# Optimization experiments

Hardware: AMD Instinct MI355X
Metric: run time of the kernel (lower is better)

The kernel has to match this reference:

```python
import jax, jax.numpy as jnp
import numpy as np

EMBED = 1024
HEADS = 16
HEAD_DIM = EMBED // HEADS
N, L = 8, 1024


def setup_inputs() -> dict:
    key = jax.random.key(0)
    ks = jax.random.split(key, 12)
    s = 1.0 / np.sqrt(EMBED)
    return {
        "values": jax.random.normal(ks[0], (N, L, EMBED), jnp.float32),
        "keys": jax.random.normal(ks[1], (N, L, EMBED), jnp.float32),
        "queries": jax.random.normal(ks[2], (N, L, EMBED), jnp.float32),
        "mask": jax.random.randint(ks[3], (N, 1, L, L), 0, 2, jnp.int32),
        "Wv": jax.random.normal(ks[4], (EMBED, EMBED), jnp.float32) * s,
        "bv": jnp.zeros((EMBED,), jnp.float32),
        "Wk": jax.random.normal(ks[5], (EMBED, EMBED), jnp.float32) * s,
        "bk": jnp.zeros((EMBED,), jnp.float32),
        "Wq": jax.random.normal(ks[6], (EMBED, EMBED), jnp.float32) * s,
        "bq": jnp.zeros((EMBED,), jnp.float32),
        "Wo": jax.random.normal(ks[7], (EMBED, EMBED), jnp.float32) * s,
        "bo": jnp.zeros((EMBED,), jnp.float32),
    }


def reference(values, keys, queries, mask, Wv, bv, Wk, bk, Wq, bq, Wo, bo):
    n, q_len = queries.shape[0], queries.shape[1]
    # Linear projections (torch Linear: x @ W.T + b)
    v = values @ Wv.T + bv
    k = keys @ Wk.T + bk
    q = queries @ Wq.T + bq
    # split heads: [N, L, H, D]
    v = v.reshape(n, -1, HEADS, HEAD_DIM)
    k = k.reshape(n, -1, HEADS, HEAD_DIM)
    q = q.reshape(n, q_len, HEADS, HEAD_DIM)
    # energy: [N, H, Q, K]
    energy = jnp.einsum("nqhd,nkhd->nhqk", q, k)
    energy = jnp.where(mask == 0, jnp.float32(-1e20), energy)
    attention = jax.nn.softmax(energy / jnp.sqrt(jnp.float32(EMBED)), axis=3)
    out = jnp.einsum("nhqk,nkhd->nqhd", attention, v).reshape(n, q_len, EMBED)
    return out @ Wo.T + bo
```

## Files before the change

### kernel.cpp

```cpp
#include <hip/hip_runtime.h>
#include <hip/hip_bf16.h>


typedef __attribute__((ext_vector_type(8))) short short8;
typedef __attribute__((ext_vector_type(8))) __bf16 bf16x8;
typedef __attribute__((ext_vector_type(4))) float f32x4;
typedef __attribute__((ext_vector_type(16))) float f32x16;
typedef __attribute__((ext_vector_type(4))) unsigned short ushort4v;

static __device__ __forceinline__ unsigned short f2bf(float x) {
  union { float f; unsigned u; } v; v.f = x;
  unsigned r = v.u + 0x7FFFu + ((v.u >> 16) & 1u);
  return (unsigned short)(r >> 16);
}

static __device__ __forceinline__ f32x4 mfma16(short8 a, short8 b, f32x4 c) {
  return __builtin_amdgcn_mfma_f32_16x16x32_bf16(
      __builtin_bit_cast(bf16x8, a), __builtin_bit_cast(bf16x8, b), c, 0, 0, 0);
}
static __device__ __forceinline__ f32x16 mfma32(short8 a, short8 b, f32x16 c) {
  return __builtin_amdgcn_mfma_f32_32x32x16_bf16(
      __builtin_bit_cast(bf16x8, a), __builtin_bit_cast(bf16x8, b), c, 0, 0, 0);
}

static __device__ __forceinline__ void gll16(const unsigned short* g, unsigned short* l) {
  __builtin_amdgcn_global_load_lds(
      (const __attribute__((address_space(1))) unsigned int*)(const void*)g,
      (__attribute__((address_space(3))) unsigned int*)(void*)l, 16, 0, 0);
}

static __device__ __forceinline__ unsigned cvtpk(float lo, float hi) {
  unsigned r;
  asm("v_cvt_pk_bf16_f32 %0, %1, %2" : "=v"(r) : "v"(lo), "v"(hi));
  return r;
}

static __device__ __forceinline__ void cvt8(const float* __restrict__ in,
                                            unsigned short* __restrict__ out, int i) {
  float4 a = ((const float4*)in)[i * 2];
  float4 b = ((const float4*)in)[i * 2 + 1];
  union { short8 v; unsigned short u[8]; } pk;
  pk.u[0] = f2bf(a.x); pk.u[1] = f2bf(a.y); pk.u[2] = f2bf(a.z); pk.u[3] = f2bf(a.w);
  pk.u[4] = f2bf(b.x); pk.u[5] = f2bf(b.y); pk.u[6] = f2bf(b.z); pk.u[7] = f2bf(b.w);
  ((short8*)out)[i] = pk.v;
}

__global__ __launch_bounds__(256)
void fused_pre(const float* __restrict__ queries, const float* __restrict__ keys,
               const float* __restrict__ Wq, const float* __restrict__ Wk,
               const float* __restrict__ Wv, const float* __restrict__ Wo,
               const int* __restrict__ mask,
               unsigned short* __restrict__ Xq, unsigned short* __restrict__ Xk,
               unsigned short* __restrict__ W4, unsigned long long* __restrict__ M64)
{
  const int bid = blockIdx.x, tid = threadIdx.x;
  if (bid < 4096) {
    cvt8(queries, Xq, bid * 256 + tid);
  } else if (bid < 8192) {
    cvt8(keys, Xk, (bid - 4096) * 256 + tid);
  } else if (bid < 10240) {
    const int wsel = (bid - 8192) >> 9;
    const float* src = wsel == 0 ? Wq : wsel == 1 ? Wk : wsel == 2 ? Wv : Wo;
    cvt8(src, W4 + wsel * 1048576, ((bid - 8192) & 511) * 256 + tid);
  } else {
    const int lane = tid & 63, wid = tid >> 6;
    const int gw = (bid - 10240) * 4 + wid;
#pragma unroll 4
    for (int j = 0; j < 32; ++j) {
      const int w = gw * 32 + j;
      unsigned long long b = __ballot(mask[(size_t)w * 64 + lane] != 0);
      if (lane == 0) M64[w] = b;
    }
  }
}

__global__ __launch_bounds__(256)
void cvt_kernel(const float* __restrict__ in, unsigned short* __restrict__ out, int n8)
{
  int i = blockIdx.x * 256 + threadIdx.x;
  if (i >= n8) return;
  cvt8(in, out, i);
}

template<int MODE>
__global__ __launch_bounds__(256)
void gemm_kernel(const unsigned short* __restrict__ A, const unsigned short* __restrict__ B,
                 const float* __restrict__ bias, void* __restrict__ outp)
{
  __shared__ alignas(16) unsigned short As[128][32];
  __shared__ alignas(16) unsigned short Bs[128][32];
  const int tid = threadIdx.x, lane = tid & 63, wid = tid >> 6;
  const int l15 = lane & 15, lg = lane >> 4;
  const int bm = blockIdx.x >> 3, bn = blockIdx.x & 7;
  const int wr = (wid >> 1) * 64, wc = (wid & 1) * 64;

  f32x4 acc[4][4] = {};
  const int o = wid * 1024 + lane * 16;
  const unsigned short* gA0 = A + (size_t)(bm * 128 + (o >> 6)) * 1024 + ((o & 63) >> 1);
  const unsigned short* gA1 = gA0 + 64 * 1024;
  const unsigned short* gB0 = B + (size_t)(bn * 128 + (o >> 6)) * 1024 + ((o & 63) >> 1);
  const unsigned short* gB1 = gB0 + 64 * 1024;
  unsigned short* lA0 = &As[0][0] + wid * 512;
  unsigned short* lA1 = lA0 + 2048;
  unsigned short* lB0 = &Bs[0][0] + wid * 512;
  unsigned short* lB1 = lB0 + 2048;

  for (int k0 = 0; k0 < 1024; k0 += 32) {
    __syncthreads();
    gll16(gA0 + k0, lA0); gll16(gA1 + k0, lA1);
    gll16(gB0 + k0, lB0); gll16(gB1 + k0, lB1);
    __syncthreads();
    short8 af[4], bf[4];
#pragma unroll
    for (int f = 0; f < 4; ++f) {
      af[f] = *(const short8*)&As[wr + f * 16 + l15][lg * 8];
      bf[f] = *(const short8*)&Bs[wc + f * 16 + l15][lg * 8];
    }
#pragma unroll
    for (int r = 0; r < 4; ++r)
#pragma unroll
      for (int c = 0; c < 4; ++c)
        acc[r][c] = mfma16(af[r], bf[c], acc[r][c]);
  }

#pragma unroll
  for (int r = 0; r < 4; ++r) {
    const int mb = bm * 128 + wr + r * 16 + lg * 4;
#pragma unroll
    for (int c = 0; c < 4; ++c) {
      const int col = bn * 128 + wc + c * 16 + l15;
      const float bv = bias[col];
      if (MODE == 0) {
        unsigned short* O = (unsigned short*)outp;
#pragma unroll
        for (int i = 0; i < 4; ++i)
          O[(size_t)(mb + i) * 1024 + col] = f2bf(acc[r][c][i] + bv);
      } else if (MODE == 1) {
        unsigned short* O = (unsigned short*)outp;
        const int n = mb >> 10, l = mb & 1023, hh = col >> 6, d = col & 63;
        union { ushort4v v; unsigned short u[4]; } pk;
#pragma unroll
        for (int i = 0; i < 4; ++i) pk.u[i] = f2bf(acc[r][c][i] + bv);
        *(ushort4v*)&O[(size_t)((n * 16 + hh) * 64 + d) * 1024 + l] = pk.v;
      } else {
        float* O = (float*)outp;
#pragma unroll
        for (int i = 0; i < 4; ++i)
          O[(size_t)(mb + i) * 1024 + col] = acc[r][c][i] + bv;
      }
    }
  }
}

__global__ __launch_bounds__(256)
void attn_kernel(const unsigned short* __restrict__ Q,
                 const unsigned short* __restrict__ K,
                 const unsigned short* __restrict__ VT,
                 const unsigned long long* __restrict__ M64,
                 unsigned short* __restrict__ AO)
{
  __shared__ alignas(16) unsigned short KV[2][8192];
  const int tid = threadIdx.x, lane = tid & 63, wid = tid >> 6;
  const int l31 = lane & 31, hi = lane >> 5, hi4 = hi * 4;
  const int w = (blockIdx.x & 7) * 128 + (blockIdx.x >> 3);
  const int qt = w & 7, nh = w >> 3, h = nh & 15, n = nh >> 4;
  const int qbase = qt * 128 + wid * 32;

  const unsigned short* src[4];
  unsigned short* dst0[4];
  int tstride;
  if (wid < 2) {
#pragma unroll
    for (int i = 0; i < 4; ++i) {
      const int g = wid * 4 + i, c = g >> 1, kh = g & 1;
      src[i] = K + ((size_t)(n * 1024 + kh * 32 + l31) << 10) + h * 64 + c * 16 + hi * 8;
      dst0[i] = &KV[0][g * 512];
    }
    tstride = 64 * 1024;
  } else {
#pragma unroll
    for (int i = 0; i < 4; ++i) {
      const int g = (wid - 2) * 4 + i, kt = g >> 1, dh = g & 1;
      src[i] = VT + ((size_t)((n * 16 + h) * 64 + dh * 32 + l31) << 10) + kt * 16 + hi * 8;
      dst0[i] = &KV[0][4096 + g * 512];
    }
    tstride = 64;
  }

  short8 qf[4];
#pragma unroll
  for (int c = 0; c < 4; ++c)
    qf[c] = *(const short8*)&Q[(size_t)(n * 1024 + qbase + l31) * 1024 + h * 64 + c * 16 + hi * 8];

  const unsigned long long* Mq = M64 + (size_t)(n * 1024 + qbase + l31) * 16;
  unsigned long long mw = Mq[0], mwn = 0;

  f32x16 oacc0 = {}, oacc1 = {}, lacc = {};
  const float SC = 0.03125f * 1.44269504089f;
  short8 ones;
#pragma unroll
  for (int j = 0; j < 8; ++j) ones[j] = (short)0x3F80;

#pragma unroll
  for (int i = 0; i < 4; ++i) gll16(src[i], dst0[i]);

  int cur = 0;
#pragma unroll 2
  for (int t = 0; t < 16; ++t) {
    __syncthreads();
    if (t < 15) {
      const size_t off = (size_t)(t + 1) * tstride;
#pragma unroll
      for (int i = 0; i < 4; ++i) gll16(src[i] + off, dst0[i] + (cur ^ 1) * 8192);
      mwn = Mq[t + 1];
    }
    const unsigned short* Kb = &KV[cur][0];

    f32x16 s0 = {}, s1 = {};
#pragma unroll
    for (int c = 0; c < 4; ++c) {
      short8 kf0 = *(const short8*)&Kb[(c * 2 + 0) * 512 + lane * 8];
      short8 kf1 = *(const short8*)&Kb[(c * 2 + 1) * 512 + lane * 8];
      s0 = mfma32(kf0, qf[c], s0);
      s1 = mfma32(kf1, qf[c], s1);
    }

    const unsigned wlo = (unsigned)mw >> hi4;
    const unsigned whi = (unsigned)(mw >> 32) >> hi4;
    short8 pa[4];
#pragma unroll
    for (int kt = 0; kt < 2; ++kt) {
      const unsigned wsh = kt ? whi : wlo;
      float p[16];
#pragma unroll
      for (int r = 0; r < 16; ++r) {
        const float pe = exp2f((kt ? s1[r] : s0[r]) * SC);
        const int pos = 8 * (r >> 2) + (r & 3);
        const int msk = ((int)(wsh << (31 - pos))) >> 31;
        p[r] = __builtin_bit_cast(float, __builtin_bit_cast(int, pe) & msk);
      }
      unsigned u[4][2];
#pragma unroll
      for (int g = 0; g < 4; ++g) {
        u[g][0] = cvtpk(p[4 * g], p[4 * g + 1]);
        u[g][1] = cvtpk(p[4 * g + 2], p[4 * g + 3]);
      }
#pragma unroll
      for (int m = 0; m < 2; ++m) {
        unsigned a0 = u[2 * m][0], b0 = u[2 * m + 1][0];
        unsigned a1 = u[2 * m][1], b1 = u[2 * m + 1][1];
        asm("v_permlane32_swap_b32 %0, %1" : "+v"(a0), "+v"(b0));
        asm("v_permlane32_swap_b32 %0, %1" : "+v"(a1), "+v"(b1));
        union { unsigned uu[4]; short8 v; } pk;
        pk.uu[0] = a0; pk.uu[1] = a1; pk.uu[2] = b0; pk.uu[3] = b1;
        pa[kt * 2 + m] = pk.v;
      }
    }

#pragma unroll
    for (int kt = 0; kt < 4; ++kt) {
      short8 vf0 = *(const short8*)&Kb[4096 + (kt * 2 + 0) * 512 + lane * 8];
      short8 vf1 = *(const short8*)&Kb[4096 + (kt * 2 + 1) * 512 + lane * 8];
      oacc0 = mfma32(pa[kt], vf0, oacc0);
      oacc1 = mfma32(pa[kt], vf1, oacc1);
      lacc  = mfma32(pa[kt], ones, lacc);
    }

    mw = mwn;
    cur ^= 1;
  }

#pragma unroll
  for (int r = 0; r < 16; ++r) {
    const int qrow = 8 * (r >> 2) + (r & 3) + hi4;
    const float rl = 1.0f / lacc[r];
    const size_t row = (size_t)(n * 1024 + qbase + qrow) * 1024 + h * 64;
    AO[row + l31]      = f2bf(oacc0[r] * rl);
    AO[row + 32 + l31] = f2bf(oacc1[r] * rl);
  }
}

extern "C" void kernel_launch(void* const* d_in, const int* in_sizes, int n_in,
                              void* d_out, int out_size, void* d_ws, size_t ws_size,
                              hipStream_t stream) {
  (void)in_sizes; (void)n_in; (void)out_size; (void)ws_size;
  const float* values  = (const float*)d_in[0];
  const float* keys    = (const float*)d_in[1];
  const float* queries = (const float*)d_in[2];
  const int*   mask    = (const int*)d_in[3];
  const float* Wv = (const float*)d_in[4];
  const float* bv = (const float*)d_in[5];
  const float* Wk = (const float*)d_in[6];
  const float* bk = (const float*)d_in[7];
  const float* Wq = (const float*)d_in[8];
  const float* bq = (const float*)d_in[9];
  const float* Wo = (const float*)d_in[10];
  const float* bo = (const float*)d_in[11];

  const size_t MB = 1u << 20;
  char* ws = (char*)d_ws;
  unsigned short* R0  = (unsigned short*)(ws);
  unsigned short* R16 = (unsigned short*)(ws + 16 * MB);
  unsigned short* Qb  = (unsigned short*)(ws + 32 * MB);
  unsigned short* Kb  = (unsigned short*)(ws + 48 * MB);
  unsigned short* W4  = (unsigned short*)(ws + 64 * MB);
  unsigned long long* M64 = (unsigned long long*)(ws + 72 * MB);

  const dim3 b256(256);
  const int NX8 = 8 * 1024 * 1024 / 8;

  fused_pre<<<dim3(11264), b256, 0, stream>>>(queries, keys, Wq, Wk, Wv, Wo, mask,
                                              R0, R16, W4, M64);
  gemm_kernel<0><<<dim3(512), b256, 0, stream>>>(R0,  W4,               bq, (void*)Qb);
  gemm_kernel<0><<<dim3(512), b256, 0, stream>>>(R16, W4 + 1048576,     bk, (void*)Kb);
  cvt_kernel<<<dim3(4096), b256, 0, stream>>>(values, R0, NX8);
  gemm_kernel<1><<<dim3(512), b256, 0, stream>>>(R0,  W4 + 2 * 1048576, bv, (void*)R16);
  attn_kernel<<<dim3(1024), b256, 0, stream>>>(Qb, Kb, R16, M64, R0 );
  gemm_kernel<2><<<dim3(512), b256, 0, stream>>>(R0,  W4 + 3 * 1048576, bo, d_out);
}
```

Before: 231.3 us.

## Pipeline attention PV with next QK, fold scale into Q, fuse values cvt

The attention loop is software-pipelined. The PV MFMAs for the previous tile run after the QK MFMAs of the current tile, with a triple-buffered V LDS ring and s_setprio hints. The row-sum MFMA against a ones vector is replaced by scalar per-lane sums combined with a shuffle and a bpermute. The softmax scale is folded into the Q projection epilogue, the values conversion moves into the fused preprocessing kernel when the workspace is large enough, and the GEMM block order is swizzled for L2 reuse. These changes add register pressure from the double-buffered probability fragments, and rounding differs slightly because the scale is applied before bf16 conversion.

After: 325.9 us. 40.9% more time.

```diff
diff --git a/kernel.cpp b/kernel.cpp
--- a/kernel.cpp
+++ b/kernel.cpp
@@ -47,10 +47,12 @@
 
 __global__ __launch_bounds__(256)
 void fused_pre(const float* __restrict__ queries, const float* __restrict__ keys,
+               const float* __restrict__ values,
                const float* __restrict__ Wq, const float* __restrict__ Wk,
                const float* __restrict__ Wv, const float* __restrict__ Wo,
                const int* __restrict__ mask,
                unsigned short* __restrict__ Xq, unsigned short* __restrict__ Xk,
+               unsigned short* __restrict__ Xv,
                unsigned short* __restrict__ W4, unsigned long long* __restrict__ M64)
 {
   const int bid = blockIdx.x, tid = threadIdx.x;
@@ -62,7 +64,7 @@
     const int wsel = (bid - 8192) >> 9;
     const float* src = wsel == 0 ? Wq : wsel == 1 ? Wk : wsel == 2 ? Wv : Wo;
     cvt8(src, W4 + wsel * 1048576, ((bid - 8192) & 511) * 256 + tid);
-  } else {
+  } else if (bid < 11264) {
     const int lane = tid & 63, wid = tid >> 6;
     const int gw = (bid - 10240) * 4 + wid;
 #pragma unroll 4
@@ -71,6 +73,8 @@
       unsigned long long b = __ballot(mask[(size_t)w * 64 + lane] != 0);
       if (lane == 0) M64[w] = b;
     }
+  } else {
+    cvt8(values, Xv, (bid - 11264) * 256 + tid);
   }
 }
 
@@ -85,13 +89,14 @@
 template<int MODE>
 __global__ __launch_bounds__(256)
 void gemm_kernel(const unsigned short* __restrict__ A, const unsigned short* __restrict__ B,
-                 const float* __restrict__ bias, void* __restrict__ outp)
+                 const float* __restrict__ bias, void* __restrict__ outp, float oscale)
 {
   __shared__ alignas(16) unsigned short As[128][32];
   __shared__ alignas(16) unsigned short Bs[128][32];
   const int tid = threadIdx.x, lane = tid & 63, wid = tid >> 6;
   const int l15 = lane & 15, lg = lane >> 4;
-  const int bm = blockIdx.x >> 3, bn = blockIdx.x & 7;
+  const int j = blockIdx.x >> 3;
+  const int bm = (blockIdx.x & 7) * 8 + (j & 7), bn = j >> 3;
   const int wr = (wid >> 1) * 64, wc = (wid & 1) * 64;
 
   f32x4 acc[4][4] = {};
@@ -134,7 +139,7 @@
         unsigned short* O = (unsigned short*)outp;
 #pragma unroll
         for (int i = 0; i < 4; ++i)
-          O[(size_t)(mb + i) * 1024 + col] = f2bf(acc[r][c][i] + bv);
+          O[(size_t)(mb + i) * 1024 + col] = f2bf((acc[r][c][i] + bv) * oscale);
       } else if (MODE == 1) {
         unsigned short* O = (unsigned short*)outp;
         const int n = mb >> 10, l = mb & 1023, hh = col >> 6, d = col & 63;
@@ -159,7 +164,8 @@
                  const unsigned long long* __restrict__ M64,
                  unsigned short* __restrict__ AO)
 {
-  __shared__ alignas(16) unsigned short KV[2][8192];
+  __shared__ alignas(16) unsigned short Kb[2][4096];
+  __shared__ alignas(16) unsigned short Vb[3][4096];
   const int tid = threadIdx.x, lane = tid & 63, wid = tid >> 6;
   const int l31 = lane & 31, hi = lane >> 5, hi4 = hi * 4;
   const int w = (blockIdx.x & 7) * 128 + (blockIdx.x >> 3);
@@ -167,24 +173,25 @@
   const int qbase = qt * 128 + wid * 32;
 
   const unsigned short* src[4];
-  unsigned short* dst0[4];
-  int tstride;
-  if (wid < 2) {
+  int ldsoff[4];
+  size_t tstep;
+  const bool isK = wid < 2;
+  if (isK) {
 #pragma unroll
     for (int i = 0; i < 4; ++i) {
       const int g = wid * 4 + i, c = g >> 1, kh = g & 1;
       src[i] = K + ((size_t)(n * 1024 + kh * 32 + l31) << 10) + h * 64 + c * 16 + hi * 8;
-      dst0[i] = &KV[0][g * 512];
-    }
-    tstride = 64 * 1024;
+      ldsoff[i] = g * 512;
+    }
+    tstep = 64 * 1024;
   } else {
 #pragma unroll
     for (int i = 0; i < 4; ++i) {
       const int g = (wid - 2) * 4 + i, kt = g >> 1, dh = g & 1;
-      src[i] = VT + ((size_t)((n * 16 + h) * 64 + dh * 32 + l31) << 10) + kt * 16 + hi * 8;
-      dst0[i] = &KV[0][4096 + g * 512];
-    }
-    tstride = 64;
+      src[i] = VT + ((size_t)(nh * 64 + dh * 32 + l31) << 10) + kt * 16 + hi * 8;
+      ldsoff[i] = g * 512;
+    }
+    tstep = 64;
   }
 
   short8 qf[4];
@@ -195,50 +202,63 @@
   const unsigned long long* Mq = M64 + (size_t)(n * 1024 + qbase + l31) * 16;
   unsigned long long mw = Mq[0], mwn = 0;
 
-  f32x16 oacc0 = {}, oacc1 = {}, lacc = {};
-  const float SC = 0.03125f * 1.44269504089f;
-  short8 ones;
-#pragma unroll
-  for (int j = 0; j < 8; ++j) ones[j] = (short)0x3F80;
-
-#pragma unroll
-  for (int i = 0; i < 4; ++i) gll16(src[i], dst0[i]);
-
-  int cur = 0;
-#pragma unroll 2
+  f32x16 oacc0 = {}, oacc1 = {};
+  float l_r = 0.f;
+  short8 pa[2][4];
+
+  {
+    unsigned short* base = isK ? &Kb[0][0] : &Vb[0][0];
+#pragma unroll
+    for (int i = 0; i < 4; ++i) gll16(src[i], base + ldsoff[i]);
+  }
+
+#pragma unroll
   for (int t = 0; t < 16; ++t) {
     __syncthreads();
     if (t < 15) {
-      const size_t off = (size_t)(t + 1) * tstride;
-#pragma unroll
-      for (int i = 0; i < 4; ++i) gll16(src[i] + off, dst0[i] + (cur ^ 1) * 8192);
+      unsigned short* base = isK ? &Kb[(t + 1) & 1][0] : &Vb[(t + 1) % 3][0];
+      const size_t off = (size_t)(t + 1) * tstep;
+#pragma unroll
+      for (int i = 0; i < 4; ++i) gll16(src[i] + off, base + ldsoff[i]);
       mwn = Mq[t + 1];
     }
-    const unsigned short* Kb = &KV[cur][0];
 
     f32x16 s0 = {}, s1 = {};
+    __builtin_amdgcn_s_setprio(1);
 #pragma unroll
     for (int c = 0; c < 4; ++c) {
-      short8 kf0 = *(const short8*)&Kb[(c * 2 + 0) * 512 + lane * 8];
-      short8 kf1 = *(const short8*)&Kb[(c * 2 + 1) * 512 + lane * 8];
+      short8 kf0 = *(const short8*)&Kb[t & 1][(c * 2 + 0) * 512 + lane * 8];
+      short8 kf1 = *(const short8*)&Kb[t & 1][(c * 2 + 1) * 512 + lane * 8];
       s0 = mfma32(kf0, qf[c], s0);
       s1 = mfma32(kf1, qf[c], s1);
     }
+    if (t > 0) {
+#pragma unroll
+      for (int kt = 0; kt < 4; ++kt) {
+        short8 vf0 = *(const short8*)&Vb[(t - 1) % 3][(kt * 2 + 0) * 512 + lane * 8];
+        short8 vf1 = *(const short8*)&Vb[(t - 1) % 3][(kt * 2 + 1) * 512 + lane * 8];
+        oacc0 = mfma32(pa[(t - 1) & 1][kt], vf0, oacc0);
+        oacc1 = mfma32(pa[(t - 1) & 1][kt], vf1, oacc1);
+      }
+    }
+    __builtin_amdgcn_s_setprio(0);
 
     const unsigned wlo = (unsigned)mw >> hi4;
     const unsigned whi = (unsigned)(mw >> 32) >> hi4;
-    short8 pa[4];
 #pragma unroll
     for (int kt = 0; kt < 2; ++kt) {
       const unsigned wsh = kt ? whi : wlo;
       float p[16];
+      float lsum = 0.f;
 #pragma unroll
       for (int r = 0; r < 16; ++r) {
-        const float pe = exp2f((kt ? s1[r] : s0[r]) * SC);
+        const float pe = exp2f(kt ? s1[r] : s0[r]);
         const int pos = 8 * (r >> 2) + (r & 3);
         const int msk = ((int)(wsh << (31 - pos))) >> 31;
         p[r] = __builtin_bit_cast(float, __builtin_bit_cast(int, pe) & msk);
-      }
+        lsum += p[r];
+      }
+      l_r += lsum;
       unsigned u[4][2];
 #pragma unroll
       for (int g = 0; g < 4; ++g) {
@@ -253,27 +273,29 @@
         asm("v_permlane32_swap_b32 %0, %1" : "+v"(a1), "+v"(b1));
         union { unsigned uu[4]; short8 v; } pk;
         pk.uu[0] = a0; pk.uu[1] = a1; pk.uu[2] = b0; pk.uu[3] = b1;
-        pa[kt * 2 + m] = pk.v;
-      }
-    }
-
-#pragma unroll
-    for (int kt = 0; kt < 4; ++kt) {
-      short8 vf0 = *(const short8*)&Kb[4096 + (kt * 2 + 0) * 512 + lane * 8];
-      short8 vf1 = *(const short8*)&Kb[4096 + (kt * 2 + 1) * 512 + lane * 8];
-      oacc0 = mfma32(pa[kt], vf0, oacc0);
-      oacc1 = mfma32(pa[kt], vf1, oacc1);
-      lacc  = mfma32(pa[kt], ones, lacc);
-    }
-
+        pa[t & 1][kt * 2 + m] = pk.v;
+      }
+    }
     mw = mwn;
-    cur ^= 1;
-  }
-
+  }
+
+  __builtin_amdgcn_s_setprio(1);
+#pragma unroll
+  for (int kt = 0; kt < 4; ++kt) {
+    short8 vf0 = *(const short8*)&Vb[0][(kt * 2 + 0) * 512 + lane * 8];
+    short8 vf1 = *(const short8*)&Vb[0][(kt * 2 + 1) * 512 + lane * 8];
+    oacc0 = mfma32(pa[1][kt], vf0, oacc0);
+    oacc1 = mfma32(pa[1][kt], vf1, oacc1);
+  }
+  __builtin_amdgcn_s_setprio(0);
+
+  const float l_tot = l_r + __shfl_xor(l_r, 32);
+  const float inv_l = 1.0f / l_tot;
+  const int invi = __builtin_bit_cast(int, inv_l);
 #pragma unroll
   for (int r = 0; r < 16; ++r) {
     const int qrow = 8 * (r >> 2) + (r & 3) + hi4;
-    const float rl = 1.0f / lacc[r];
+    const float rl = __builtin_bit_cast(float, __builtin_amdgcn_ds_bpermute(qrow * 4, invi));
     const size_t row = (size_t)(n * 1024 + qbase + qrow) * 1024 + h * 64;
     AO[row + l31]      = f2bf(oacc0[r] * rl);
     AO[row + 32 + l31] = f2bf(oacc1[r] * rl);
@@ -283,7 +305,7 @@
 extern "C" void kernel_launch(void* const* d_in, const int* in_sizes, int n_in,
                               void* d_out, int out_size, void* d_ws, size_t ws_size,
                               hipStream_t stream) {
-  (void)in_sizes; (void)n_in; (void)out_size; (void)ws_size;
+  (void)in_sizes; (void)n_in; (void)out_size;
   const float* values  = (const float*)d_in[0];
   const float* keys    = (const float*)d_in[1];
   const float* queries = (const float*)d_in[2];
@@ -305,16 +327,21 @@
   unsigned short* Kb  = (unsigned short*)(ws + 48 * MB);
   unsigned short* W4  = (unsigned short*)(ws + 64 * MB);
   unsigned long long* M64 = (unsigned long long*)(ws + 72 * MB);
+  unsigned short* Xv  = (unsigned short*)(ws + 73 * MB);
+  const bool foldv = ws_size >= 90 * MB;
 
   const dim3 b256(256);
   const int NX8 = 8 * 1024 * 1024 / 8;
-
-  fused_pre<<<dim3(11264), b256, 0, stream>>>(queries, keys, Wq, Wk, Wv, Wo, mask,
-                                              R0, R16, W4, M64);
-  gemm_kernel<0><<<dim3(512), b256, 0, stream>>>(R0,  W4,               bq, (void*)Qb);
-  gemm_kernel<0><<<dim3(512), b256, 0, stream>>>(R16, W4 + 1048576,     bk, (void*)Kb);
-  cvt_kernel<<<dim3(4096), b256, 0, stream>>>(values, R0, NX8);
-  gemm_kernel<1><<<dim3(512), b256, 0, stream>>>(R0,  W4 + 2 * 1048576, bv, (void*)R16);
+  const float SCFULL = 0.03125f * 1.44269504089f;
+
+  fused_pre<<<dim3(foldv ? 15360 : 11264), b256, 0, stream>>>(
+      queries, keys, values, Wq, Wk, Wv, Wo, mask, R0, R16, Xv, W4, M64);
+  gemm_kernel<0><<<dim3(512), b256, 0, stream>>>(R0,  W4,               bq, (void*)Qb, SCFULL);
+  gemm_kernel<0><<<dim3(512), b256, 0, stream>>>(R16, W4 + 1048576,     bk, (void*)Kb, 1.0f);
+  if (!foldv)
+    cvt_kernel<<<dim3(4096), b256, 0, stream>>>(values, R0, NX8);
+  gemm_kernel<1><<<dim3(512), b256, 0, stream>>>(foldv ? Xv : R0, W4 + 2 * 1048576,
+                                                 bv, (void*)R16, 1.0f);
   attn_kernel<<<dim3(1024), b256, 0, stream>>>(Qb, Kb, R16, M64, R0 );
-  gemm_kernel<2><<<dim3(512), b256, 0, stream>>>(R0,  W4 + 3 * 1048576, bo, d_out);
-}
+  gemm_kernel<2><<<dim3(512), b256, 0, stream>>>(R0, W4 + 3 * 1048576, bo, d_out, 1.0f);
+}
```
